# Kernel optimization log

Hardware: AMD Instinct MI355X
Metric: run time of the kernel (lower is better)

## Reference

```python
import jax, jax.numpy as jnp
import numpy as np

NUM_CHUNKS = 8
TOP_K = 2
IN_F = 4096
HID_F = 4096
OUT_F = 4096
B = 4096


def setup_inputs() -> dict:
    key = jax.random.key(0)
    k = jax.random.split(key, 5)
    cin = IN_F // NUM_CHUNKS    # 512
    cout = HID_F // NUM_CHUNKS  # 512
    s_in = 1.0 / np.sqrt(cin)
    s_fin = 1.0 / np.sqrt(cout * TOP_K)
    return {
        "x": jax.random.normal(k[0], (B, IN_F), dtype=jnp.float32),
        # stacked chunk-expert Linear params: y = x @ W + b
        "W_chunks": jax.random.uniform(k[1], (NUM_CHUNKS, cin, cout), jnp.float32, -s_in, s_in),
        "b_chunks": jax.random.uniform(k[2], (NUM_CHUNKS, cout), jnp.float32, -s_in, s_in),
        "W_final": jax.random.uniform(k[3], (cout * TOP_K, OUT_F), jnp.float32, -s_fin, s_fin),
        "b_final": jax.random.uniform(k[4], (OUT_F,), jnp.float32, -s_fin, s_fin),
    }


def reference(x, W_chunks, b_chunks, W_final, b_final):
    Bsz = x.shape[0]
    # split into chunks along feature dim: (B, num_chunks, chunk_in)
    xr = x.reshape(Bsz, NUM_CHUNKS, -1)
    # per-chunk activity = mean(|chunk|) over the whole batch (matches torch .abs().mean())
    activities = jnp.mean(jnp.abs(xr), axis=(0, 2))  # (num_chunks,)
    _, topk_idx = jax.lax.top_k(activities, TOP_K)    # descending, like torch.topk
    # gather selected chunks and their expert weights, run small GEMMs
    x_sel = xr[:, topk_idx, :]                        # (B, k, chunk_in)
    h = jnp.einsum('bkc,kcd->bkd', x_sel, W_chunks[topk_idx]) + b_chunks[topk_idx]
    h = h.reshape(Bsz, -1)                            # concat along feature dim
    out = h @ W_final + b_final                       # (B, out_features)
    return out
```

## Files before the change

### kernel.cpp

```cpp
#include <hip/hip_runtime.h>


typedef __bf16 bf16x8_t __attribute__((ext_vector_type(8)));
typedef float  f32x4_t  __attribute__((ext_vector_type(4)));

__device__ inline unsigned short f2bf(float f) {
    __bf16 b = (__bf16)f;
    return __builtin_bit_cast(unsigned short, b);
}

__device__ inline void stage_glds(const unsigned short* gtile, int stride, int row0,
                                  unsigned short* lds, int lane) {
    const int r8 = lane >> 3;
    const int gg = (lane & 7) ^ r8;
    const unsigned short* gp = gtile + (size_t)(row0 + r8) * stride + gg * 8;
    unsigned short* lp = lds + row0 * 64;
    __builtin_amdgcn_global_load_lds((const __attribute__((address_space(1))) void*)gp,
                                     (__attribute__((address_space(3))) void*)lp,
                                     16, 0, 0);
}

__device__ inline bf16x8_t ldsfrag(const unsigned short* Ls, int row, int kb) {
    return *(const bf16x8_t*)(Ls + row * 64 + (((kb >> 3) ^ (row & 7)) * 8));
}

__global__ void activity_topk_kernel(const float* __restrict__ x, float* __restrict__ act,
                                     int* __restrict__ counter, int* __restrict__ idxg) {
    const int b = blockIdx.x;
    const int chunk = b & 7;
    const int rg = b >> 3;
    const int tid = threadIdx.x;
    const int colf4 = tid & 127;
    const int rsub = tid >> 7;
    const float4* base = (const float4*)x + (size_t)chunk * 128 + colf4;
    float s = 0.f;
    #pragma unroll 4
    for (int i = 0; i < 32; ++i) {
        int row = rg * 64 + i * 2 + rsub;
        float4 v = base[(size_t)row * 1024];
        s += fabsf(v.x) + fabsf(v.y) + fabsf(v.z) + fabsf(v.w);
    }
    #pragma unroll
    for (int off = 32; off > 0; off >>= 1) s += __shfl_down(s, off, 64);
    __shared__ float wsum[4];
    if ((tid & 63) == 0) wsum[tid >> 6] = s;
    __syncthreads();
    if (tid == 0) {
        atomicAdd(&act[chunk], wsum[0] + wsum[1] + wsum[2] + wsum[3]);
        __threadfence();
        int old = atomicAdd(counter, 1);
        if (old == gridDim.x - 1) {
            float v0 = -1e30f, v1 = -1e30f; int b0 = 0, b1 = 0;
            for (int i = 0; i < 8; ++i) {
                float v = atomicAdd(&act[i], 0.0f);
                if (v > v0) { v1 = v0; b1 = b0; v0 = v; b0 = i; }
                else if (v > v1) { v1 = v; b1 = i; }
            }
            idxg[0] = b0; idxg[1] = b1;
            __threadfence();
        }
    }
}

__global__ void prep_kernel(const float* __restrict__ x, const float* __restrict__ Wc,
                            const float* __restrict__ Wf, const int* __restrict__ idxg,
                            unsigned short* __restrict__ xsel, unsigned short* __restrict__ wct,
                            unsigned short* __restrict__ wft) {
    const int j = blockIdx.x;
    const int tid = threadIdx.x;
    if (j < 4096) {
        const int c = tid * 4;
        const int z = c >> 9;
        const int sc = idxg[z] * 512 + (c & 511);
        float4 v = *(const float4*)(x + (size_t)j * 4096 + sc);
        ushort4 o;
        o.x = f2bf(v.x); o.y = f2bf(v.y); o.z = f2bf(v.z); o.w = f2bf(v.w);
        *(ushort4*)(xsel + (size_t)j * 1024 + c) = o;
        return;
    }
    __shared__ float tile[32][33];
    const int tx = tid & 31, ty = tid >> 5;
    const float* src; unsigned short* dst; int R, C, cb, rb;
    if (j < 8192) {
        int jj = j - 4096;
        src = Wf; dst = wft; R = 1024; C = 4096;
        cb = (jj & 127) * 32; rb = (jj >> 7) * 32;
    } else {
        int jj = j - 8192;
        int z = jj >> 8, t = jj & 255;
        src = Wc + (size_t)idxg[z] * 262144;
        dst = wct + (size_t)z * 262144;
        R = 512; C = 512;
        cb = (t & 15) * 32; rb = (t >> 4) * 32;
    }
    #pragma unroll
    for (int i = 0; i < 4; ++i)
        tile[ty + i * 8][tx] = src[(size_t)(rb + ty + i * 8) * C + cb + tx];
    __syncthreads();
    #pragma unroll
    for (int i = 0; i < 4; ++i)
        dst[(size_t)(cb + ty + i * 8) * R + rb + tx] = f2bf(tile[tx][ty + i * 8]);
}

__global__ __launch_bounds__(256, 4)
void gemm1_kernel(const unsigned short* __restrict__ xsel, const unsigned short* __restrict__ wct,
                  const float* __restrict__ bc, const int* __restrict__ idxg,
                  unsigned short* __restrict__ h) {
    __shared__ __align__(16) unsigned short As[64 * 64];
    __shared__ __align__(16) unsigned short Bs[128 * 64];
    const int z = blockIdx.z;
    const int idxz = idxg[z];
    const int m0 = blockIdx.x * 64;
    const int n0 = blockIdx.y * 128;
    const int tid = threadIdx.x;
    const int wave = tid >> 6;
    const int lane = tid & 63;
    const int wm = (wave >> 1) * 32;
    const int wn = (wave & 1) * 64;
    const int rl = lane & 15;
    const int quad = lane >> 4;

    const unsigned short* Atile = xsel + (size_t)m0 * 1024 + z * 512;
    const unsigned short* Btile = wct + (size_t)z * 262144 + (size_t)n0 * 512;

    f32x4_t acc[2][4] = {};

    for (int k0 = 0; k0 < 512; k0 += 64) {
        #pragma unroll
        for (int s = wave; s < 24; s += 4) {
            if (s < 8) stage_glds(Atile + k0, 1024, s * 8, As, lane);
            else       stage_glds(Btile + k0, 512, (s - 8) * 8, Bs, lane);
        }
        __syncthreads();
        #pragma unroll
        for (int kq = 0; kq < 2; ++kq) {
            const int kb = kq * 32 + quad * 8;
            bf16x8_t af[2], bfr[4];
            #pragma unroll
            for (int i = 0; i < 2; ++i) af[i]  = ldsfrag(As, wm + i * 16 + rl, kb);
            #pragma unroll
            for (int i = 0; i < 4; ++i) bfr[i] = ldsfrag(Bs, wn + i * 16 + rl, kb);
            #pragma unroll
            for (int mi = 0; mi < 2; ++mi)
                #pragma unroll
                for (int ni = 0; ni < 4; ++ni)
                    acc[mi][ni] = __builtin_amdgcn_mfma_f32_16x16x32_bf16(af[mi], bfr[ni], acc[mi][ni], 0, 0, 0);
        }
        __syncthreads();
    }

    const int row_l = quad * 4;
    const float* bias = bc + (size_t)idxz * 512;
    #pragma unroll
    for (int ni = 0; ni < 4; ++ni) {
        int col = n0 + wn + ni * 16 + rl;
        float bv = bias[col];
        #pragma unroll
        for (int mi = 0; mi < 2; ++mi) {
            #pragma unroll
            for (int j = 0; j < 4; ++j) {
                int row = m0 + wm + mi * 16 + row_l + j;
                h[(size_t)row * 1024 + z * 512 + col] = f2bf(acc[mi][ni][j] + bv);
            }
        }
    }
}

__global__ __launch_bounds__(256, 3)
void gemm2_kernel(const unsigned short* __restrict__ h, const unsigned short* __restrict__ wft,
                  const float* __restrict__ bfin, float* __restrict__ out) {
    __shared__ __align__(16) unsigned short As[128 * 64];
    __shared__ __align__(16) unsigned short Bs[128 * 64];
    const int m0 = blockIdx.x * 128;
    const int n0 = blockIdx.y * 128;
    const int tid = threadIdx.x;
    const int wave = tid >> 6;
    const int lane = tid & 63;
    const int wm = (wave >> 1) * 64;
    const int wn = (wave & 1) * 64;
    const int rl = lane & 15;
    const int quad = lane >> 4;

    const unsigned short* Atile = h + (size_t)m0 * 1024;
    const unsigned short* Btile = wft + (size_t)n0 * 1024;

    f32x4_t acc[4][4] = {};

    for (int k0 = 0; k0 < 1024; k0 += 64) {
        #pragma unroll
        for (int s = wave; s < 32; s += 4) {
            if (s < 16) stage_glds(Atile + k0, 1024, s * 8, As, lane);
            else        stage_glds(Btile + k0, 1024, (s - 16) * 8, Bs, lane);
        }
        __syncthreads();
        #pragma unroll
        for (int kq = 0; kq < 2; ++kq) {
            const int kb = kq * 32 + quad * 8;
            bf16x8_t af[4], bfr[4];
            #pragma unroll
            for (int i = 0; i < 4; ++i) {
                af[i]  = ldsfrag(As, wm + i * 16 + rl, kb);
                bfr[i] = ldsfrag(Bs, wn + i * 16 + rl, kb);
            }
            #pragma unroll
            for (int mi = 0; mi < 4; ++mi)
                #pragma unroll
                for (int ni = 0; ni < 4; ++ni)
                    acc[mi][ni] = __builtin_amdgcn_mfma_f32_16x16x32_bf16(af[mi], bfr[ni], acc[mi][ni], 0, 0, 0);
        }
        __syncthreads();
    }

    const int row_l = quad * 4;
    float bv[4];
    #pragma unroll
    for (int ni = 0; ni < 4; ++ni) bv[ni] = bfin[n0 + wn + ni * 16 + rl];
    #pragma unroll
    for (int mi = 0; mi < 4; ++mi) {
        #pragma unroll
        for (int ni = 0; ni < 4; ++ni) {
            int col = n0 + wn + ni * 16 + rl;
            #pragma unroll
            for (int j = 0; j < 4; ++j) {
                int row = m0 + wm + mi * 16 + row_l + j;
                out[(size_t)row * 4096 + col] = acc[mi][ni][j] + bv[ni];
            }
        }
    }
}

extern "C" void kernel_launch(void* const* d_in, const int* in_sizes, int n_in,
                              void* d_out, int out_size, void* d_ws, size_t ws_size,
                              hipStream_t stream) {
    const float* x    = (const float*)d_in[0];
    const float* Wc   = (const float*)d_in[1];
    const float* bc   = (const float*)d_in[2];
    const float* Wf   = (const float*)d_in[3];
    const float* bfin = (const float*)d_in[4];
    float* out = (float*)d_out;

    float* act     = (float*)d_ws;
    int*   counter = (int*)((char*)d_ws + 64);
    int*   idxg    = (int*)((char*)d_ws + 128);
    unsigned short* xsel = (unsigned short*)((char*)d_ws + 4096);
    unsigned short* h    = xsel + (size_t)4096 * 1024;
    unsigned short* wct  = h    + (size_t)4096 * 1024;
    unsigned short* wft  = wct  + (size_t)2 * 512 * 512;

    hipMemsetAsync(d_ws, 0, 128, stream);

    activity_topk_kernel<<<512, 256, 0, stream>>>(x, act, counter, idxg);
    prep_kernel<<<8704, 256, 0, stream>>>(x, Wc, Wf, idxg, xsel, wct, wft);
    gemm1_kernel<<<dim3(64, 4, 2), 256, 0, stream>>>(xsel, wct, bc, idxg, h);
    gemm2_kernel<<<dim3(32, 32, 1), 256, 0, stream>>>(h, wft, bfin, out);
}
```

Before: 215.7 us.

## Fuse activity reduction with weight prep and convert x inside gemm1

Merges the activity-reduction kernel into the weight-transpose prep kernel, writing per-block partial sums instead of atomics. All eight chunk weights are transposed to bf16 so prep no longer has to wait on the top-k result. Each gemm1 block re-reduces the partials and picks the top-2 itself, then loads fp32 x directly and converts it to bf16 into LDS, which drops the xsel staging buffer, the memset and one launch. The cost is converting four times more chunk weights, redundant top-k work in every gemm1 block, and register-based A loads instead of direct-to-LDS loads, with launch bounds lowered to 2.

Result: faster. 185.3 us (-14.1%).

```diff
diff --git a/kernel.cpp b/kernel.cpp
--- a/kernel.cpp
+++ b/kernel.cpp
@@ -24,72 +24,46 @@
     return *(const bf16x8_t*)(Ls + row * 64 + (((kb >> 3) ^ (row & 7)) * 8));
 }
 
-__global__ void activity_topk_kernel(const float* __restrict__ x, float* __restrict__ act,
-                                     int* __restrict__ counter, int* __restrict__ idxg) {
+__global__ void fused_prep_kernel(const float* __restrict__ x, const float* __restrict__ Wc,
+                                  const float* __restrict__ Wf, float* __restrict__ part,
+                                  unsigned short* __restrict__ wct, unsigned short* __restrict__ wft) {
     const int b = blockIdx.x;
-    const int chunk = b & 7;
-    const int rg = b >> 3;
     const int tid = threadIdx.x;
-    const int colf4 = tid & 127;
-    const int rsub = tid >> 7;
-    const float4* base = (const float4*)x + (size_t)chunk * 128 + colf4;
-    float s = 0.f;
-    #pragma unroll 4
-    for (int i = 0; i < 32; ++i) {
-        int row = rg * 64 + i * 2 + rsub;
-        float4 v = base[(size_t)row * 1024];
-        s += fabsf(v.x) + fabsf(v.y) + fabsf(v.z) + fabsf(v.w);
-    }
-    #pragma unroll
-    for (int off = 32; off > 0; off >>= 1) s += __shfl_down(s, off, 64);
-    __shared__ float wsum[4];
-    if ((tid & 63) == 0) wsum[tid >> 6] = s;
-    __syncthreads();
-    if (tid == 0) {
-        atomicAdd(&act[chunk], wsum[0] + wsum[1] + wsum[2] + wsum[3]);
-        __threadfence();
-        int old = atomicAdd(counter, 1);
-        if (old == gridDim.x - 1) {
-            float v0 = -1e30f, v1 = -1e30f; int b0 = 0, b1 = 0;
-            for (int i = 0; i < 8; ++i) {
-                float v = atomicAdd(&act[i], 0.0f);
-                if (v > v0) { v1 = v0; b1 = b0; v0 = v; b0 = i; }
-                else if (v > v1) { v1 = v; b1 = i; }
-            }
-            idxg[0] = b0; idxg[1] = b1;
-            __threadfence();
-        }
-    }
-}
-
-__global__ void prep_kernel(const float* __restrict__ x, const float* __restrict__ Wc,
-                            const float* __restrict__ Wf, const int* __restrict__ idxg,
-                            unsigned short* __restrict__ xsel, unsigned short* __restrict__ wct,
-                            unsigned short* __restrict__ wft) {
-    const int j = blockIdx.x;
-    const int tid = threadIdx.x;
-    if (j < 4096) {
-        const int c = tid * 4;
-        const int z = c >> 9;
-        const int sc = idxg[z] * 512 + (c & 511);
-        float4 v = *(const float4*)(x + (size_t)j * 4096 + sc);
-        ushort4 o;
-        o.x = f2bf(v.x); o.y = f2bf(v.y); o.z = f2bf(v.z); o.w = f2bf(v.w);
-        *(ushort4*)(xsel + (size_t)j * 1024 + c) = o;
+
+    if (b < 512) {
+        const int chunk = b & 7;
+        const int rg = b >> 3;
+        const int colf4 = tid & 127;
+        const int rsub = tid >> 7;
+        const float4* base = (const float4*)x + (size_t)chunk * 128 + colf4;
+        float s = 0.f;
+        #pragma unroll 4
+        for (int i = 0; i < 32; ++i) {
+            int row = rg * 64 + i * 2 + rsub;
+            float4 v = base[(size_t)row * 1024];
+            s += fabsf(v.x) + fabsf(v.y) + fabsf(v.z) + fabsf(v.w);
+        }
+        #pragma unroll
+        for (int off = 32; off > 0; off >>= 1) s += __shfl_down(s, off, 64);
+        __shared__ float wsum[4];
+        if ((tid & 63) == 0) wsum[tid >> 6] = s;
+        __syncthreads();
+        if (tid == 0) part[chunk * 64 + rg] = wsum[0] + wsum[1] + wsum[2] + wsum[3];
         return;
     }
+
     __shared__ float tile[32][33];
     const int tx = tid & 31, ty = tid >> 5;
     const float* src; unsigned short* dst; int R, C, cb, rb;
-    if (j < 8192) {
-        int jj = j - 4096;
+    int jj = b - 512;
+    if (jj < 4096) {
         src = Wf; dst = wft; R = 1024; C = 4096;
         cb = (jj & 127) * 32; rb = (jj >> 7) * 32;
     } else {
-        int jj = j - 8192;
-        int z = jj >> 8, t = jj & 255;
-        src = Wc + (size_t)idxg[z] * 262144;
-        dst = wct + (size_t)z * 262144;
+        jj -= 4096;
+        int c = jj >> 8, t = jj & 255;
+        src = Wc + (size_t)c * 262144;
+        dst = wct + (size_t)c * 262144;
         R = 512; C = 512;
         cb = (t & 15) * 32; rb = (t >> 4) * 32;
     }
@@ -102,34 +76,76 @@
         dst[(size_t)(cb + ty + i * 8) * R + rb + tx] = f2bf(tile[tx][ty + i * 8]);
 }
 
-__global__ __launch_bounds__(256, 4)
-void gemm1_kernel(const unsigned short* __restrict__ xsel, const unsigned short* __restrict__ wct,
-                  const float* __restrict__ bc, const int* __restrict__ idxg,
+__global__ __launch_bounds__(256, 2)
+void gemm1_kernel(const float* __restrict__ x, const unsigned short* __restrict__ wct,
+                  const float* __restrict__ bc, const float* __restrict__ part,
                   unsigned short* __restrict__ h) {
-    __shared__ __align__(16) unsigned short As[64 * 64];
-    __shared__ __align__(16) unsigned short Bs[128 * 64];
-    const int z = blockIdx.z;
-    const int idxz = idxg[z];
-    const int m0 = blockIdx.x * 64;
-    const int n0 = blockIdx.y * 128;
+    __shared__ __align__(16) unsigned char lds_raw[24576];
+    unsigned short* As = (unsigned short*)lds_raw;
+    unsigned short* Bs = (unsigned short*)(lds_raw + 8192);
+
     const int tid = threadIdx.x;
     const int wave = tid >> 6;
     const int lane = tid & 63;
+
+    {
+        float* sred = (float*)lds_raw;
+        sred[tid] = part[tid];
+        sred[tid + 256] = part[tid + 256];
+        __syncthreads();
+        float* act8 = (float*)(lds_raw + 2048);
+        if (tid < 8) {
+            float a = 0.f;
+            #pragma unroll
+            for (int k = 0; k < 64; ++k) a += sred[tid * 64 + k];
+            act8[tid] = a;
+        }
+        __syncthreads();
+    }
+    int sel0, sel1;
+    {
+        const float* act8 = (const float*)(lds_raw + 2048);
+        float v0 = -1e30f, v1 = -1e30f; int b0 = 0, b1 = 0;
+        #pragma unroll
+        for (int i = 0; i < 8; ++i) {
+            float v = act8[i];
+            if (v > v0) { v1 = v0; b1 = b0; v0 = v; b0 = i; }
+            else if (v > v1) { v1 = v; b1 = i; }
+        }
+        sel0 = b0; sel1 = b1;
+    }
+    __syncthreads();
+
+    const int z = blockIdx.z;
+    const int idxz = z ? sel1 : sel0;
+    const int m0 = blockIdx.x * 64;
+    const int n0 = blockIdx.y * 128;
     const int wm = (wave >> 1) * 32;
     const int wn = (wave & 1) * 64;
     const int rl = lane & 15;
     const int quad = lane >> 4;
 
-    const unsigned short* Atile = xsel + (size_t)m0 * 1024 + z * 512;
-    const unsigned short* Btile = wct + (size_t)z * 262144 + (size_t)n0 * 512;
+    const float* xtile = x + (size_t)m0 * 4096 + idxz * 512;
+    const unsigned short* Btile = wct + (size_t)idxz * 262144 + (size_t)n0 * 512;
 
     f32x4_t acc[2][4] = {};
+    const int ar = tid >> 2;
+    const int aq = tid & 3;
 
     for (int k0 = 0; k0 < 512; k0 += 64) {
         #pragma unroll
-        for (int s = wave; s < 24; s += 4) {
-            if (s < 8) stage_glds(Atile + k0, 1024, s * 8, As, lane);
-            else       stage_glds(Btile + k0, 512, (s - 8) * 8, Bs, lane);
+        for (int s = wave; s < 16; s += 4)
+            stage_glds(Btile + k0, 512, s * 8, Bs, lane);
+        const float* gr = xtile + (size_t)ar * 4096 + k0;
+        #pragma unroll
+        for (int j = 0; j < 2; ++j) {
+            int gg = aq * 2 + j;
+            float4 a = *(const float4*)(gr + gg * 8);
+            float4 c = *(const float4*)(gr + gg * 8 + 4);
+            bf16x8_t v;
+            v[0] = (__bf16)a.x; v[1] = (__bf16)a.y; v[2] = (__bf16)a.z; v[3] = (__bf16)a.w;
+            v[4] = (__bf16)c.x; v[5] = (__bf16)c.y; v[6] = (__bf16)c.z; v[7] = (__bf16)c.w;
+            *(bf16x8_t*)(As + ar * 64 + ((gg ^ (ar & 7)) * 8)) = v;
         }
         __syncthreads();
         #pragma unroll
@@ -239,18 +255,12 @@
     const float* bfin = (const float*)d_in[4];
     float* out = (float*)d_out;
 
-    float* act     = (float*)d_ws;
-    int*   counter = (int*)((char*)d_ws + 64);
-    int*   idxg    = (int*)((char*)d_ws + 128);
-    unsigned short* xsel = (unsigned short*)((char*)d_ws + 4096);
-    unsigned short* h    = xsel + (size_t)4096 * 1024;
-    unsigned short* wct  = h    + (size_t)4096 * 1024;
-    unsigned short* wft  = wct  + (size_t)2 * 512 * 512;
-
-    hipMemsetAsync(d_ws, 0, 128, stream);
-
-    activity_topk_kernel<<<512, 256, 0, stream>>>(x, act, counter, idxg);
-    prep_kernel<<<8704, 256, 0, stream>>>(x, Wc, Wf, idxg, xsel, wct, wft);
-    gemm1_kernel<<<dim3(64, 4, 2), 256, 0, stream>>>(xsel, wct, bc, idxg, h);
+    float* part = (float*)d_ws;
+    unsigned short* h   = (unsigned short*)((char*)d_ws + 4096);
+    unsigned short* wct = h   + (size_t)4096 * 1024;
+    unsigned short* wft = wct + (size_t)8 * 512 * 512;
+
+    fused_prep_kernel<<<6656, 256, 0, stream>>>(x, Wc, Wf, part, wct, wft);
+    gemm1_kernel<<<dim3(64, 4, 2), 256, 0, stream>>>(x, wct, bc, part, h);
     gemm2_kernel<<<dim3(32, 32, 1), 256, 0, stream>>>(h, wft, bfin, out);
 }
```
